# Optimization experiments

Hardware: AMD Instinct MI355X
Metric: run time of the kernel (lower is better)

The kernel has to match this reference:

```python
import jax, jax.numpy as jnp
import numpy as np

D_MODEL = 1024
EXPAND = 2
D_INNER = EXPAND * D_MODEL      # 2048
D_STATE = 2
D_CONV = 4
DT_RANK = (D_MODEL + 15) // 16  # 64
BATCH, SEQ = 2, 4096
LN_EPS = 1e-5


def setup_inputs() -> dict:
    key = jax.random.key(0)
    ks = jax.random.split(key, 16)
    s = 0.02
    inp = {
        "x":       jax.random.normal(ks[0], (BATCH, SEQ, D_MODEL), jnp.float32),
        # Mamba params (torch Linear convention: W is [out, in])
        "w_in":    jax.random.normal(ks[1], (2 * D_INNER, D_MODEL), jnp.float32) * s,
        "conv_w":  jax.random.normal(ks[2], (D_INNER, 1, D_CONV), jnp.float32) * s,
        "conv_b":  jnp.zeros((D_INNER,), jnp.float32),
        "w_xproj": jax.random.normal(ks[3], (DT_RANK + 2 * D_STATE, D_INNER), jnp.float32) * s,
        "w_dt":    jax.random.normal(ks[4], (D_INNER, DT_RANK), jnp.float32) * s,
        "b_dt":    jax.random.normal(ks[5], (D_INNER,), jnp.float32) * s - 4.0,  # softplus -> small dt
        "a_log":   jnp.log(jnp.broadcast_to(jnp.arange(1, D_STATE + 1, dtype=jnp.float32), (D_INNER, D_STATE))),
        "d_skip":  jnp.ones((D_INNER,), jnp.float32),
        "w_out":   jax.random.normal(ks[6], (D_MODEL, D_INNER), jnp.float32) * s,
        # LayerNorms
        "ln1_g":   jnp.ones((D_MODEL,), jnp.float32),
        "ln1_b":   jnp.zeros((D_MODEL,), jnp.float32),
        "ln2_g":   jnp.ones((D_MODEL,), jnp.float32),
        "ln2_b":   jnp.zeros((D_MODEL,), jnp.float32),
        # FFN (Linear d->d, ReLU, Linear d->d; dropout inactive at eval)
        "ffn_w1":  jax.random.normal(ks[7], (D_MODEL, D_MODEL), jnp.float32) * s,
        "ffn_b1":  jnp.zeros((D_MODEL,), jnp.float32),
        "ffn_w2":  jax.random.normal(ks[8], (D_MODEL, D_MODEL), jnp.float32) * s,
        "ffn_b2":  jnp.zeros((D_MODEL,), jnp.float32),
    }
    return inp


def _ln(x, g, b):
    mu = x.mean(-1, keepdims=True)
    v = ((x - mu) ** 2).mean(-1, keepdims=True)
    return (x - mu) * jax.lax.rsqrt(v + LN_EPS) * g + b


def _mamba(x, w_in, conv_w, conv_b, w_xproj, w_dt, b_dt, a_log, d_skip, w_out):
    Bsz = x.shape[0]
    xz = x @ w_in.T                      # (B,L,2*D_INNER)
    xp, z = jnp.split(xz, 2, axis=-1)
    # depthwise causal conv over time
    xc = jnp.transpose(xp, (0, 2, 1))    # (B,D,L)
    xc = jax.lax.conv_general_dilated(
        xc, conv_w, window_strides=(1,), padding=[(D_CONV - 1, 0)],
        feature_group_count=D_INNER)
    xc = xc + conv_b[None, :, None]
    xp = jax.nn.silu(jnp.transpose(xc, (0, 2, 1)))   # (B,L,D)
    # input-dependent SSM params
    x_dbl = xp @ w_xproj.T               # (B,L,DT_RANK+2N)
    dt, Bm, Cm = jnp.split(x_dbl, [DT_RANK, DT_RANK + D_STATE], axis=-1)
    dt = jax.nn.softplus(dt @ w_dt.T + b_dt)          # (B,L,D)
    A = -jnp.exp(a_log)                  # (D,N)
    dA = jnp.exp(dt[..., None] * A)                  # (B,L,D,N)
    dBu = dt[..., None] * Bm[:, :, None, :] * xp[..., None]  # (B,L,D,N)

    def step(h, inp):
        da, dbu, c = inp                 # (B,D,N),(B,D,N),(B,N)
        h = da * h + dbu
        y = jnp.einsum('bdn,bn->bd', h, c)
        return h, y

    h0 = jnp.zeros((Bsz, D_INNER, D_STATE), x.dtype)
    _, ys = jax.lax.scan(step, h0, (jnp.swapaxes(dA, 0, 1),
                                    jnp.swapaxes(dBu, 0, 1),
                                    jnp.swapaxes(Cm, 0, 1)))
    y = jnp.swapaxes(ys, 0, 1)           # (B,L,D)
    y = (y + d_skip * xp) * jax.nn.silu(z)
    return y @ w_out.T                   # (B,L,d_model)


def reference(x, w_in, conv_w, conv_b, w_xproj, w_dt, b_dt, a_log, d_skip, w_out,
              ln1_g, ln1_b, ln2_g, ln2_b, ffn_w1, ffn_b1, ffn_w2, ffn_b2):
    h = x + _mamba(_ln(x, ln1_g, ln1_b), w_in, conv_w, conv_b, w_xproj,
                   w_dt, b_dt, a_log, d_skip, w_out)
    f = _ln(h, ln2_g, ln2_b)
    f = jax.nn.relu(f @ ffn_w1.T + ffn_b1) @ ffn_w2.T + ffn_b2
    return h + f
```

## Files before the change

kernel.cpp:

```cpp
#include <hip/hip_runtime.h>

typedef unsigned short u16;
typedef __bf16 bf16x8 __attribute__((ext_vector_type(8)));
typedef float f32x4 __attribute__((ext_vector_type(4)));

#define SEQ   4096
#define DM    1024
#define DI    2048
#define NTOK  8192
#define NXP   68
#define DTR   64
#define NCH   4096
#define CHUNK 64
#define NCHK  64

__device__ __forceinline__ float bf2f(u16 v) {
  union { unsigned u; float f; } x; x.u = ((unsigned)v) << 16; return x.f;
}
__device__ __forceinline__ u16 f2bf(float f) {
  unsigned u = __float_as_uint(f);
  return (u16)((u + 0x7FFFu + ((u >> 16) & 1u)) >> 16);
}

__device__ __forceinline__ void g2l16(const u16* g, u16* l) {
  __builtin_amdgcn_global_load_lds(
      (const __attribute__((address_space(1))) unsigned int*)g,
      (__attribute__((address_space(3))) unsigned int*)l, 16, 0, 0);
}

__global__ __launch_bounds__(256)
void detect_kernel(const u16* __restrict__ x, int* __restrict__ flag)
{
  __shared__ int tot;
  if (threadIdx.x == 0) tot = 0;
  __syncthreads();
  int cnt = 0;
  for (int i = threadIdx.x; i < 4096; i += 256) {
    const int e = (x[2 * i] >> 7) & 0xFF;
    if (e > 167) cnt++;
  }
  atomicAdd(&tot, cnt);
  __syncthreads();
  if (threadIdx.x == 0) flag[0] = (tot >= 8) ? 1 : 0;
}

__global__ __launch_bounds__(256)
void convert_kernel(const void* __restrict__ src, u16* __restrict__ dst, int n,
                    const int* __restrict__ flag)
{
  const int i = blockIdx.x * 256 + threadIdx.x;
  if (i < n)
    dst[i] = (*flag) ? f2bf(((const float*)src)[i]) : ((const u16*)src)[i];
}

__global__ __launch_bounds__(256)
void convert_small_kernel(const void* s0, const void* s1, const void* s2,
                          const void* s3, const void* s4, const void* s5,
                          const void* s6, const void* s7, const void* s8,
                          const void* s9, const void* s10,
                          u16* __restrict__ dst, const int* __restrict__ flag)
{
  const int i = blockIdx.x * 256 + threadIdx.x;
  if (i >= 24576) return;
  const void* src; int off;
  if      (i < 8192)  { src = s0;  off = i; }
  else if (i < 10240) { src = s1;  off = i - 8192; }
  else if (i < 12288) { src = s2;  off = i - 10240; }
  else if (i < 16384) { src = s3;  off = i - 12288; }
  else if (i < 18432) { src = s4;  off = i - 16384; }
  else if (i < 19456) { src = s5;  off = i - 18432; }
  else if (i < 20480) { src = s6;  off = i - 19456; }
  else if (i < 21504) { src = s7;  off = i - 20480; }
  else if (i < 22528) { src = s8;  off = i - 21504; }
  else if (i < 23552) { src = s9;  off = i - 22528; }
  else                { src = s10; off = i - 23552; }
  dst[i] = (*flag) ? f2bf(((const float*)src)[off]) : ((const u16*)src)[off];
}

template<bool DUAL>
__global__ __launch_bounds__(256)
void ln_kernel(const void* __restrict__ xin, const u16* __restrict__ gw,
               const u16* __restrict__ bw, u16* __restrict__ outp,
               const int* __restrict__ flag)
{
  const int row = blockIdx.x;
  const int tid = threadIdx.x;
  const bool isf32 = DUAL ? (*flag != 0) : true;
  const float* xf = (const float*)xin;
  const u16*   xb = (const u16*)xin;
  float v[4];
#pragma unroll
  for (int k = 0; k < 4; ++k) {
    size_t idx = (size_t)row * DM + tid + k * 256;
    v[k] = isf32 ? xf[idx] : bf2f(xb[idx]);
  }
  float s = v[0] + v[1] + v[2] + v[3];
  float s2 = v[0]*v[0] + v[1]*v[1] + v[2]*v[2] + v[3]*v[3];
#pragma unroll
  for (int off = 32; off > 0; off >>= 1) {
    s  += __shfl_down(s,  off);
    s2 += __shfl_down(s2, off);
  }
  __shared__ float red[8];
  const int wv = tid >> 6, lane = tid & 63;
  if (lane == 0) { red[wv] = s; red[4 + wv] = s2; }
  __syncthreads();
  if (tid == 0) {
    float ts = red[0] + red[1] + red[2] + red[3];
    float t2 = red[4] + red[5] + red[6] + red[7];
    float mu = ts * (1.f / DM);
    float var = t2 * (1.f / DM) - mu * mu;
    red[0] = mu; red[1] = rsqrtf(var + 1e-5f);
  }
  __syncthreads();
  const float mu = red[0], rs = red[1];
#pragma unroll
  for (int k = 0; k < 4; ++k) {
    int col = tid + k * 256;
    size_t idx = (size_t)row * DM + col;
    outp[idx] = f2bf((v[k] - mu) * rs * bf2f(gw[col]) + bf2f(bw[col]));
  }
}

template<int EPI, int LNBX>
__global__ __launch_bounds__(256, 2)
void gemm_kernel(const u16* __restrict__ A, const u16* __restrict__ B,
                 int M, int N, int K,
                 const u16* __restrict__ bias, const u16* __restrict__ addbf,
                 const float* __restrict__ addf, const int* __restrict__ dtflag,
                 void* __restrict__ Cp)
{
  __shared__ __align__(16) u16 sA[128 * 32];
  __shared__ __align__(16) u16 sB[128 * 32];
  const int tid = threadIdx.x;
  const int b = blockIdx.x;
  const int xcd = b & 7;
  const int kk = b >> 3;
  const int bx = kk & ((1 << LNBX) - 1);
  const int by = xcd * 8 + (kk >> LNBX);
  const int m0 = by * 128;
  const int n0 = bx * 128;
  const int lane = tid & 63;
  const int wv = tid >> 6;
  const int wm = (wv & 1) * 64;
  const int wn = (wv >> 1) * 64;
  const int r = lane & 15;
  const int q = lane >> 4;

  const int pr = lane >> 2;
  const int pk = (lane & 3) * 8;
  u16* lA0 = &sA[(wv * 2 + 0) * 512];
  u16* lA1 = &sA[(wv * 2 + 1) * 512];
  u16* lB0 = &sB[(wv * 2 + 0) * 512];
  u16* lB1 = &sB[(wv * 2 + 1) * 512];
  const u16* gA0 = A + (size_t)(m0 + wv * 32 + pr) * K + pk;
  const u16* gA1 = gA0 + (size_t)16 * K;
  const u16* gB0 = B + (size_t)(n0 + wv * 32 + pr) * K + pk;
  const u16* gB1 = gB0 + (size_t)16 * K;

  const int fl = (EPI == 3 || EPI == 5) ? *dtflag : 0;

  f32x4 acc[4][4];
#pragma unroll
  for (int i = 0; i < 4; ++i)
#pragma unroll
    for (int j = 0; j < 4; ++j)
#pragma unroll
      for (int t = 0; t < 4; ++t) acc[i][j][t] = 0.f;

  const int nk = K >> 5;
  for (int kt = 0; kt < nk; ++kt) {
    g2l16(gA0, lA0); g2l16(gA1, lA1);
    g2l16(gB0, lB0); g2l16(gB1, lB1);
    gA0 += 32; gA1 += 32; gB0 += 32; gB1 += 32;
    __syncthreads();
    bf16x8 af[4], bfr[4];
#pragma unroll
    for (int i = 0; i < 4; ++i)
      af[i] = *reinterpret_cast<const bf16x8*>(&sA[(wm + i * 16 + r) * 32 + q * 8]);
#pragma unroll
    for (int j = 0; j < 4; ++j)
      bfr[j] = *reinterpret_cast<const bf16x8*>(&sB[(wn + j * 16 + r) * 32 + q * 8]);
#pragma unroll
    for (int i = 0; i < 4; ++i)
#pragma unroll
      for (int j = 0; j < 4; ++j)
        acc[i][j] = __builtin_amdgcn_mfma_f32_16x16x32_bf16(af[i], bfr[j], acc[i][j], 0, 0, 0);
    __syncthreads();
  }

#pragma unroll
  for (int i = 0; i < 4; ++i) {
#pragma unroll
    for (int j = 0; j < 4; ++j) {
#pragma unroll
      for (int t = 0; t < 4; ++t) {
        const int row = m0 + wm + i * 16 + q * 4 + t;
        const int col = n0 + wn + j * 16 + r;
        const size_t idx = (size_t)row * N + col;
        float v = acc[i][j][t];
        if (EPI == 1) {
          ((u16*)Cp)[idx] = f2bf(v);
        } else if (EPI == 2) {
          v += bf2f(bias[col]);
          v = (v > 15.f) ? v : __logf(1.f + __expf(v));
          ((u16*)Cp)[idx] = f2bf(v);
        } else if (EPI == 3) {
          v += fl ? addf[idx] : bf2f(addbf[idx]);
          ((float*)Cp)[idx] = v;
        } else if (EPI == 4) {
          v += bf2f(bias[col]);
          ((u16*)Cp)[idx] = f2bf(fmaxf(v, 0.f));
        } else {
          v += bf2f(bias[col]) + addf[idx];
          if (fl) ((float*)Cp)[idx] = v;
          else    ((u16*)Cp)[idx] = f2bf(v);
        }
      }
    }
  }
}

__global__ __launch_bounds__(256, 2)
void xproj_splitk(const u16* __restrict__ A, const u16* __restrict__ B,
                  float* __restrict__ part)
{
  __shared__ __align__(16) u16 sA[128 * 32];
  __shared__ __align__(16) u16 sB[128 * 32];
  const int tid = threadIdx.x;
  const int kz = blockIdx.x;
  const int m0 = blockIdx.y * 128;
  const int kbase = kz * 256;
  const int lane = tid & 63;
  const int wv = tid >> 6;
  const int wm = (wv & 1) * 64;
  const int wn = (wv >> 1) * 64;
  const int r = lane & 15;
  const int q = lane >> 4;
  const int pr = lane >> 2;
  const int pk = (lane & 3) * 8;

  u16* lA0 = &sA[(wv * 2 + 0) * 512];
  u16* lA1 = &sA[(wv * 2 + 1) * 512];
  u16* lB0 = &sB[(wv * 2 + 0) * 512];
  u16* lB1 = &sB[(wv * 2 + 1) * 512];
  int br0 = wv * 32 + pr;      if (br0 > 67) br0 = 67;
  int br1 = wv * 32 + 16 + pr; if (br1 > 67) br1 = 67;
  const u16* gA0 = A + (size_t)(m0 + wv * 32 + pr) * DI + kbase + pk;
  const u16* gA1 = gA0 + (size_t)16 * DI;
  const u16* gB0 = B + (size_t)br0 * DI + kbase + pk;
  const u16* gB1 = B + (size_t)br1 * DI + kbase + pk;

  f32x4 acc[4][4];
#pragma unroll
  for (int i = 0; i < 4; ++i)
#pragma unroll
    for (int j = 0; j < 4; ++j)
#pragma unroll
      for (int t = 0; t < 4; ++t) acc[i][j][t] = 0.f;

  for (int kt = 0; kt < 8; ++kt) {
    g2l16(gA0, lA0); g2l16(gA1, lA1);
    g2l16(gB0, lB0); g2l16(gB1, lB1);
    gA0 += 32; gA1 += 32; gB0 += 32; gB1 += 32;
    __syncthreads();
    bf16x8 af[4], bfr[4];
#pragma unroll
    for (int i = 0; i < 4; ++i)
      af[i] = *reinterpret_cast<const bf16x8*>(&sA[(wm + i * 16 + r) * 32 + q * 8]);
#pragma unroll
    for (int j = 0; j < 4; ++j)
      bfr[j] = *reinterpret_cast<const bf16x8*>(&sB[(wn + j * 16 + r) * 32 + q * 8]);
#pragma unroll
    for (int i = 0; i < 4; ++i)
#pragma unroll
      for (int j = 0; j < 4; ++j)
        acc[i][j] = __builtin_amdgcn_mfma_f32_16x16x32_bf16(af[i], bfr[j], acc[i][j], 0, 0, 0);
    __syncthreads();
  }

#pragma unroll
  for (int i = 0; i < 4; ++i)
#pragma unroll
    for (int j = 0; j < 4; ++j)
#pragma unroll
      for (int t = 0; t < 4; ++t) {
        const int row = m0 + wm + i * 16 + q * 4 + t;
        const int col = wn + j * 16 + r;
        if (col < NXP)
          part[((size_t)kz * NTOK + row) * NXP + col] = acc[i][j][t];
      }
}

__global__ __launch_bounds__(256)
void xreduce_kernel(const float* __restrict__ part, u16* __restrict__ dtraw,
                    float* __restrict__ bc)
{
  const int i = blockIdx.x * 256 + threadIdx.x;
  if (i >= NTOK * NXP) return;
  const int row = i / NXP, col = i - row * NXP;
  float s = 0.f;
#pragma unroll
  for (int z = 0; z < 8; ++z) s += part[(size_t)z * NTOK * NXP + i];
  if (col < DTR) dtraw[(size_t)row * DTR + col] = f2bf(s);
  else           bc[row * 4 + (col - DTR)] = s;
}

__global__ __launch_bounds__(256)
void conv_silu_kernel(const u16* __restrict__ xp, const u16* __restrict__ cw,
                      const u16* __restrict__ cb, u16* __restrict__ u)
{
  const int i = blockIdx.x * 256 + threadIdx.x;
  const int d = i & (DI - 1);
  const int token = i >> 11;
  const int t = token & (SEQ - 1);
  float acc = bf2f(cb[d]);
#pragma unroll
  for (int j = 0; j < 4; ++j) {
    const int tt = t - 3 + j;
    if (tt >= 0)
      acc += bf2f(cw[d * 4 + j]) * bf2f(xp[(size_t)(token - 3 + j) * DI + d]);
  }
  const float sg = 1.f / (1.f + __expf(-acc));
  u[i] = f2bf(acc * sg);
}

__global__ __launch_bounds__(256)
void scan_pass1(const u16* __restrict__ dtb, const u16* __restrict__ ub,
                const float* __restrict__ bc, const u16* __restrict__ a_log,
                float* __restrict__ S, float* __restrict__ hf0, float* __restrict__ hf1)
{
  const int g = blockIdx.x * 256 + threadIdx.x;
  const int ch = g & (NCH - 1);
  const int c = g >> 12;
  const int b = ch >> 11;
  const int d = ch & (DI - 1);
  const float A0 = -__expf(bf2f(a_log[d * 2 + 0]));
  const float A1 = -__expf(bf2f(a_log[d * 2 + 1]));
  float h0 = 0.f, h1 = 0.f, s = 0.f;
  const int row0 = b * SEQ + c * CHUNK;
  for (int i = 0; i < CHUNK; ++i) {
    const size_t row = row0 + i;
    const float dt = bf2f(dtb[row * DI + d]);
    const float uu = bf2f(ub[row * DI + d]);
    const float B0 = bc[row * 4 + 0];
    const float B1 = bc[row * 4 + 1];
    const float dtu = dt * uu;
    h0 = __expf(A0 * dt) * h0 + dtu * B0;
    h1 = __expf(A1 * dt) * h1 + dtu * B1;
    s += dt;
  }
  S[g] = s; hf0[g] = h0; hf1[g] = h1;
}

__global__ __launch_bounds__(256)
void scan_pass2(const float* __restrict__ S, const float* __restrict__ hf0,
                const float* __restrict__ hf1, const u16* __restrict__ a_log,
                float* __restrict__ hi0, float* __restrict__ hi1)
{
  const int ch = blockIdx.x * 256 + threadIdx.x;
  const int d = ch & (DI - 1);
  const float A0 = -__expf(bf2f(a_log[d * 2 + 0]));
  const float A1 = -__expf(bf2f(a_log[d * 2 + 1]));
  float h0 = 0.f, h1 = 0.f;
  for (int c = 0; c < NCHK; ++c) {
    const int g = c * NCH + ch;
    hi0[g] = h0; hi1[g] = h1;
    const float s = S[g];
    h0 = __expf(A0 * s) * h0 + hf0[g];
    h1 = __expf(A1 * s) * h1 + hf1[g];
  }
}

__global__ __launch_bounds__(256)
void scan_pass3(const u16* __restrict__ dtb, const u16* __restrict__ ub,
                const float* __restrict__ bc, const u16* __restrict__ zbuf,
                const u16* __restrict__ a_log, const u16* __restrict__ d_skip,
                const float* __restrict__ hi0, const float* __restrict__ hi1,
                u16* __restrict__ yb)
{
  const int g = blockIdx.x * 256 + threadIdx.x;
  const int ch = g & (NCH - 1);
  const int c = g >> 12;
  const int b = ch >> 11;
  const int d = ch & (DI - 1);
  const float A0 = -__expf(bf2f(a_log[d * 2 + 0]));
  const float A1 = -__expf(bf2f(a_log[d * 2 + 1]));
  const float dsk = bf2f(d_skip[d]);
  float h0 = hi0[g], h1 = hi1[g];
  const int row0 = b * SEQ + c * CHUNK;
  for (int i = 0; i < CHUNK; ++i) {
    const size_t row = row0 + i;
    const float dt = bf2f(dtb[row * DI + d]);
    const float uu = bf2f(ub[row * DI + d]);
    const float B0 = bc[row * 4 + 0];
    const float B1 = bc[row * 4 + 1];
    const float C0 = bc[row * 4 + 2];
    const float C1 = bc[row * 4 + 3];
    const float dtu = dt * uu;
    h0 = __expf(A0 * dt) * h0 + dtu * B0;
    h1 = __expf(A1 * dt) * h1 + dtu * B1;
    const float y = h0 * C0 + h1 * C1;
    const float z = bf2f(zbuf[row * DI + d]);
    const float sz = z / (1.f + __expf(-z));
    yb[row * DI + d] = f2bf((y + dsk * uu) * sz);
  }
}

extern "C" void kernel_launch(void* const* d_in, const int* in_sizes, int n_in,
                              void* d_out, int out_size, void* d_ws, size_t ws_size,
                              hipStream_t stream)
{
  const void* x       = d_in[0];
  const void* w_in    = d_in[1];
  const void* conv_w  = d_in[2];
  const void* conv_b  = d_in[3];
  const void* w_xproj = d_in[4];
  const void* w_dt    = d_in[5];
  const void* b_dt    = d_in[6];
  const void* a_log   = d_in[7];
  const void* d_skip  = d_in[8];
  const void* w_out   = d_in[9];
  const void* ln1_g   = d_in[10];
  const void* ln1_b   = d_in[11];
  const void* ln2_g   = d_in[12];
  const void* ln2_b   = d_in[13];
  const void* ffn_w1  = d_in[14];
  const void* ffn_b1  = d_in[15];
  const void* ffn_w2  = d_in[16];
  const void* ffn_b2  = d_in[17];
  char* ws = (char*)d_ws;

  const size_t o_flag  = 0;
  const size_t o_small = 256;
  const size_t o_cwout = o_small + 65536;
  const size_t o_cff1  = o_cwout + (size_t)DM * DI * 2;
  const size_t o_cff2  = o_cff1  + (size_t)DM * DM * 2;
  const size_t o_cxp   = o_cff2  + (size_t)DM * DM * 2;
  const size_t o_cwdt  = o_cxp   + (size_t)NXP * DI * 2;
  const size_t o_xn    = 9437184;
  const size_t o_xp    = o_xn + (size_t)NTOK * DM * 2;
  const size_t o_z     = o_xp + (size_t)NTOK * DI * 2;
  const size_t o_u     = o_z  + (size_t)NTOK * DI * 2;
  const size_t o_bc    = o_u  + (size_t)NTOK * DI * 2;
  const size_t o_S     = o_bc + (size_t)NTOK * 4 * 4 + 2097152;
  const size_t o_hf0   = o_S   + (size_t)NCHK * NCH * 4;
  const size_t o_hf1   = o_hf0 + (size_t)NCHK * NCH * 4;
  const size_t o_hi0   = o_hf1 + (size_t)NCHK * NCH * 4;
  const size_t o_hi1   = o_hi0 + (size_t)NCHK * NCH * 4;

  int*   flagp   = (int*)(ws + o_flag);
  u16*   csmall  = (u16*)(ws + o_small);
  u16*   c_convw = csmall +     0;
  u16*   c_convb = csmall +  8192;
  u16*   c_bdt   = csmall + 10240;
  u16*   c_alog  = csmall + 12288;
  u16*   c_dskip = csmall + 16384;
  u16*   c_ln1g  = csmall + 18432;
  u16*   c_ln1b  = csmall + 19456;
  u16*   c_ln2g  = csmall + 20480;
  u16*   c_ln2b  = csmall + 21504;
  u16*   c_fb1   = csmall + 22528;
  u16*   c_fb2   = csmall + 23552;
  u16*   c_wout  = (u16*)(ws + o_cwout);
  u16*   c_ff1   = (u16*)(ws + o_cff1);
  u16*   c_ff2   = (u16*)(ws + o_cff2);
  u16*   c_xproj = (u16*)(ws + o_cxp);
  u16*   c_wdt   = (u16*)(ws + o_cwdt);
  u16*   c_win   = (u16*)(ws + o_u);
  u16*   xn      = (u16*)(ws + o_xn);
  u16*   xp      = (u16*)(ws + o_xp);
  u16*   zb      = (u16*)(ws + o_z);
  u16*   u       = (u16*)(ws + o_u);
  float* part    = (float*)(ws + o_xp);
  u16*   dtraw   = (u16*)(ws + o_xn);
  u16*   dtb     = xp;
  u16*   yb      = xp;
  float* bc      = (float*)(ws + o_bc);
  float* S       = (float*)(ws + o_S);
  float* hf0     = (float*)(ws + o_hf0);
  float* hf1     = (float*)(ws + o_hf1);
  float* hi0     = (float*)(ws + o_hi0);
  float* hi1     = (float*)(ws + o_hi1);
  float* h       = (float*)(ws + o_z);
  u16*   hn      = (u16*)(ws + o_xn);
  u16*   f1      = (u16*)(ws + o_u);

  const dim3 blk(256);

  detect_kernel<<<1, blk, 0, stream>>>((const u16*)x, flagp);
  convert_kernel<<<(2 * DI * DM) / 256, blk, 0, stream>>>(w_in, c_win, 2 * DI * DM, flagp);
  convert_kernel<<<(NXP * DI + 255) / 256, blk, 0, stream>>>(w_xproj, c_xproj, NXP * DI, flagp);
  convert_kernel<<<(DI * DTR) / 256, blk, 0, stream>>>(w_dt, c_wdt, DI * DTR, flagp);
  convert_kernel<<<(DM * DI) / 256, blk, 0, stream>>>(w_out, c_wout, DM * DI, flagp);
  convert_kernel<<<(DM * DM) / 256, blk, 0, stream>>>(ffn_w1, c_ff1, DM * DM, flagp);
  convert_kernel<<<(DM * DM) / 256, blk, 0, stream>>>(ffn_w2, c_ff2, DM * DM, flagp);
  convert_small_kernel<<<96, blk, 0, stream>>>(conv_w, conv_b, b_dt, a_log, d_skip,
                                               ln1_g, ln1_b, ln2_g, ln2_b, ffn_b1, ffn_b2,
                                               csmall, flagp);

  ln_kernel<true><<<NTOK, blk, 0, stream>>>(x, c_ln1g, c_ln1b, xn, flagp);
  gemm_kernel<1, 4><<<1024, blk, 0, stream>>>(xn, c_win, NTOK, DI, DM,
                                              nullptr, nullptr, nullptr, flagp, xp);
  gemm_kernel<1, 4><<<1024, blk, 0, stream>>>(xn, c_win + (size_t)DI * DM, NTOK, DI, DM,
                                              nullptr, nullptr, nullptr, flagp, zb);
  conv_silu_kernel<<<NTOK * DI / 256, blk, 0, stream>>>(xp, c_convw, c_convb, u);
  xproj_splitk<<<dim3(8, 64), blk, 0, stream>>>(u, c_xproj, part);
  xreduce_kernel<<<(NTOK * NXP + 255) / 256, blk, 0, stream>>>(part, dtraw, bc);
  gemm_kernel<2, 4><<<1024, blk, 0, stream>>>(dtraw, c_wdt, NTOK, DI, DTR,
                                              c_bdt, nullptr, nullptr, flagp, dtb);
  scan_pass1<<<NCHK * NCH / 256, blk, 0, stream>>>(dtb, u, bc, c_alog, S, hf0, hf1);
  scan_pass2<<<NCH / 256, blk, 0, stream>>>(S, hf0, hf1, c_alog, hi0, hi1);
  scan_pass3<<<NCHK * NCH / 256, blk, 0, stream>>>(dtb, u, bc, zb, c_alog, c_dskip,
                                                   hi0, hi1, yb);
  gemm_kernel<3, 3><<<512, blk, 0, stream>>>(yb, c_wout, NTOK, DM, DI,
                                             nullptr, (const u16*)x, (const float*)x,
                                             flagp, h);
  ln_kernel<false><<<NTOK, blk, 0, stream>>>(h, c_ln2g, c_ln2b, hn, flagp);
  gemm_kernel<4, 3><<<512, blk, 0, stream>>>(hn, c_ff1, NTOK, DM, DM,
                                             c_fb1, nullptr, nullptr, flagp, f1);
  gemm_kernel<5, 3><<<512, blk, 0, stream>>>(f1, c_ff2, NTOK, DM, DM,
                                             c_fb2, nullptr, h, flagp, d_out);
}
```

Before: 524.4 us.

## Double-buffer LDS tiles in GEMM and x-proj split-K kernels

Both the generic GEMM kernel and the x-projection split-K kernel now keep two LDS buffers per operand. The first K-tile is loaded before the loop, and inside the loop the next tile's global-to-LDS copy is issued after the current fragments are read and before the MFMA block. The intent is to overlap global memory latency with matrix math and to drop one barrier per K step. In exchange, LDS use per block doubles, which may limit how many blocks fit on a CU under the 2-block launch bound.

```diff
diff --git a/kernel.cpp b/kernel.cpp
--- a/kernel.cpp
+++ b/kernel.cpp
@@ -130,8 +130,8 @@
                  const float* __restrict__ addf, const int* __restrict__ dtflag,
                  void* __restrict__ Cp)
 {
-  __shared__ __align__(16) u16 sA[128 * 32];
-  __shared__ __align__(16) u16 sB[128 * 32];
+  __shared__ __align__(16) u16 sA[2][128 * 32];
+  __shared__ __align__(16) u16 sB[2][128 * 32];
   const int tid = threadIdx.x;
   const int b = blockIdx.x;
   const int xcd = b & 7;
@@ -149,10 +149,10 @@
 
   const int pr = lane >> 2;
   const int pk = (lane & 3) * 8;
-  u16* lA0 = &sA[(wv * 2 + 0) * 512];
-  u16* lA1 = &sA[(wv * 2 + 1) * 512];
-  u16* lB0 = &sB[(wv * 2 + 0) * 512];
-  u16* lB1 = &sB[(wv * 2 + 1) * 512];
+  u16* lA0[2] = { &sA[0][(wv * 2 + 0) * 512], &sA[1][(wv * 2 + 0) * 512] };
+  u16* lA1[2] = { &sA[0][(wv * 2 + 1) * 512], &sA[1][(wv * 2 + 1) * 512] };
+  u16* lB0[2] = { &sB[0][(wv * 2 + 0) * 512], &sB[1][(wv * 2 + 0) * 512] };
+  u16* lB1[2] = { &sB[0][(wv * 2 + 1) * 512], &sB[1][(wv * 2 + 1) * 512] };
   const u16* gA0 = A + (size_t)(m0 + wv * 32 + pr) * K + pk;
   const u16* gA1 = gA0 + (size_t)16 * K;
   const u16* gB0 = B + (size_t)(n0 + wv * 32 + pr) * K + pk;
@@ -168,25 +168,30 @@
 #pragma unroll
       for (int t = 0; t < 4; ++t) acc[i][j][t] = 0.f;
 
+  g2l16(gA0, lA0[0]); g2l16(gA1, lA1[0]);
+  g2l16(gB0, lB0[0]); g2l16(gB1, lB1[0]);
+
   const int nk = K >> 5;
   for (int kt = 0; kt < nk; ++kt) {
-    g2l16(gA0, lA0); g2l16(gA1, lA1);
-    g2l16(gB0, lB0); g2l16(gB1, lB1);
-    gA0 += 32; gA1 += 32; gB0 += 32; gB1 += 32;
+    const int cur = kt & 1;
     __syncthreads();
     bf16x8 af[4], bfr[4];
 #pragma unroll
     for (int i = 0; i < 4; ++i)
-      af[i] = *reinterpret_cast<const bf16x8*>(&sA[(wm + i * 16 + r) * 32 + q * 8]);
+      af[i] = *reinterpret_cast<const bf16x8*>(&sA[cur][(wm + i * 16 + r) * 32 + q * 8]);
 #pragma unroll
     for (int j = 0; j < 4; ++j)
-      bfr[j] = *reinterpret_cast<const bf16x8*>(&sB[(wn + j * 16 + r) * 32 + q * 8]);
+      bfr[j] = *reinterpret_cast<const bf16x8*>(&sB[cur][(wn + j * 16 + r) * 32 + q * 8]);
+    if (kt + 1 < nk) {
+      gA0 += 32; gA1 += 32; gB0 += 32; gB1 += 32;
+      g2l16(gA0, lA0[cur ^ 1]); g2l16(gA1, lA1[cur ^ 1]);
+      g2l16(gB0, lB0[cur ^ 1]); g2l16(gB1, lB1[cur ^ 1]);
+    }
 #pragma unroll
     for (int i = 0; i < 4; ++i)
 #pragma unroll
       for (int j = 0; j < 4; ++j)
         acc[i][j] = __builtin_amdgcn_mfma_f32_16x16x32_bf16(af[i], bfr[j], acc[i][j], 0, 0, 0);
-    __syncthreads();
   }
 
 #pragma unroll
@@ -225,8 +230,8 @@
 void xproj_splitk(const u16* __restrict__ A, const u16* __restrict__ B,
                   float* __restrict__ part)
 {
-  __shared__ __align__(16) u16 sA[128 * 32];
-  __shared__ __align__(16) u16 sB[128 * 32];
+  __shared__ __align__(16) u16 sA[2][128 * 32];
+  __shared__ __align__(16) u16 sB[2][128 * 32];
   const int tid = threadIdx.x;
   const int kz = blockIdx.x;
   const int m0 = blockIdx.y * 128;
@@ -240,10 +245,10 @@
   const int pr = lane >> 2;
   const int pk = (lane & 3) * 8;
 
-  u16* lA0 = &sA[(wv * 2 + 0) * 512];
-  u16* lA1 = &sA[(wv * 2 + 1) * 512];
-  u16* lB0 = &sB[(wv * 2 + 0) * 512];
-  u16* lB1 = &sB[(wv * 2 + 1) * 512];
+  u16* lA0[2] = { &sA[0][(wv * 2 + 0) * 512], &sA[1][(wv * 2 + 0) * 512] };
+  u16* lA1[2] = { &sA[0][(wv * 2 + 1) * 512], &sA[1][(wv * 2 + 1) * 512] };
+  u16* lB0[2] = { &sB[0][(wv * 2 + 0) * 512], &sB[1][(wv * 2 + 0) * 512] };
+  u16* lB1[2] = { &sB[0][(wv * 2 + 1) * 512], &sB[1][(wv * 2 + 1) * 512] };
   int br0 = wv * 32 + pr;      if (br0 > 67) br0 = 67;
   int br1 = wv * 32 + 16 + pr; if (br1 > 67) br1 = 67;
   const u16* gA0 = A + (size_t)(m0 + wv * 32 + pr) * DI + kbase + pk;
@@ -259,24 +264,29 @@
 #pragma unroll
       for (int t = 0; t < 4; ++t) acc[i][j][t] = 0.f;
 
+  g2l16(gA0, lA0[0]); g2l16(gA1, lA1[0]);
+  g2l16(gB0, lB0[0]); g2l16(gB1, lB1[0]);
+
   for (int kt = 0; kt < 8; ++kt) {
-    g2l16(gA0, lA0); g2l16(gA1, lA1);
-    g2l16(gB0, lB0); g2l16(gB1, lB1);
-    gA0 += 32; gA1 += 32; gB0 += 32; gB1 += 32;
+    const int cur = kt & 1;
     __syncthreads();
     bf16x8 af[4], bfr[4];
 #pragma unroll
     for (int i = 0; i < 4; ++i)
-      af[i] = *reinterpret_cast<const bf16x8*>(&sA[(wm + i * 16 + r) * 32 + q * 8]);
+      af[i] = *reinterpret_cast<const bf16x8*>(&sA[cur][(wm + i * 16 + r) * 32 + q * 8]);
 #pragma unroll
     for (int j = 0; j < 4; ++j)
-      bfr[j] = *reinterpret_cast<const bf16x8*>(&sB[(wn + j * 16 + r) * 32 + q * 8]);
+      bfr[j] = *reinterpret_cast<const bf16x8*>(&sB[cur][(wn + j * 16 + r) * 32 + q * 8]);
+    if (kt + 1 < 8) {
+      gA0 += 32; gA1 += 32; gB0 += 32; gB1 += 32;
+      g2l16(gA0, lA0[cur ^ 1]); g2l16(gA1, lA1[cur ^ 1]);
+      g2l16(gB0, lB0[cur ^ 1]); g2l16(gB1, lB1[cur ^ 1]);
+    }
 #pragma unroll
     for (int i = 0; i < 4; ++i)
 #pragma unroll
       for (int j = 0; j < 4; ++j)
         acc[i][j] = __builtin_amdgcn_mfma_f32_16x16x32_bf16(af[i], bfr[j], acc[i][j], 0, 0, 0);
-    __syncthreads();
   }
 
 #pragma unroll
```

Result: no change. 517.7 us (-1.3%).
